# Performance work log

Hardware: AMD Instinct MI355X
Metric: run time of the kernel (lower is better)

Reference implementation:

```python
import jax, jax.numpy as jnp
import numpy as np

B, T, HID, NH = 2, 2048, 1024, 16
HD = HID // NH  # head_dim = 64
ROPE_BASE = 1000000.0


def _precompute_freqs(dim, end, rope_base):
    inv = 1.0 / (rope_base ** (np.arange(0, dim, 2)[: dim // 2].astype(np.float32) / dim))
    t = np.arange(end, dtype=np.float32)
    freqs = np.outer(t, inv).astype(np.float32)  # (end, dim//2)
    cos = np.concatenate([np.cos(freqs), np.cos(freqs)], axis=-1)
    sin = np.concatenate([np.sin(freqs), np.sin(freqs)], axis=-1)
    return jnp.asarray(cos), jnp.asarray(sin)


def setup_inputs() -> dict:
    key = jax.random.key(0)
    ks = jax.random.split(key, 5)
    x = jax.random.normal(ks[0], (B, T, HID), dtype=jnp.float32)
    s = 1.0 / np.sqrt(HID)
    Wq = jax.random.normal(ks[1], (HID, HID), dtype=jnp.float32) * s
    Wk = jax.random.normal(ks[2], (HID, HID), dtype=jnp.float32) * s
    Wv = jax.random.normal(ks[3], (HID, HID), dtype=jnp.float32) * s
    Wo = jax.random.normal(ks[4], (HID, HID), dtype=jnp.float32) * s
    cos, sin = _precompute_freqs(HD, T, ROPE_BASE)
    return {"x": x, "Wq": Wq, "Wk": Wk, "Wv": Wv, "Wo": Wo, "cos": cos, "sin": sin}


def _rotate_half(u):
    half = u.shape[-1] // 2
    return jnp.concatenate([-u[..., half:], u[..., :half]], axis=-1)


def reference(x, Wq, Wk, Wv, Wo, cos, sin):
    b, t, _ = x.shape
    # projections (nn.Linear: x @ W.T)
    q = (x @ Wq.T).reshape(b, t, NH, HD).transpose(0, 2, 1, 3)  # (B,H,T,D)
    k = (x @ Wk.T).reshape(b, t, NH, HD).transpose(0, 2, 1, 3)
    v = (x @ Wv.T).reshape(b, t, NH, HD).transpose(0, 2, 1, 3)
    c = cos[None, None, :t, :]
    s = sin[None, None, :t, :]
    q = q * c + _rotate_half(q) * s
    k = k * c + _rotate_half(k) * s
    scores = jnp.einsum("bhqd,bhkd->bhqk", q, k) / jnp.sqrt(jnp.float32(HD))
    causal = jnp.tril(jnp.ones((t, t), dtype=bool))
    scores = jnp.where(causal[None, None], scores, jnp.float32(-jnp.inf))
    prob = jax.nn.softmax(scores, axis=-1)
    out = jnp.einsum("bhqk,bhkd->bhqd", prob, v)
    out = out.transpose(0, 2, 1, 3).reshape(b, t, HID)
    return out @ Wo.T
```

## Files before the change

kernel.cpp:

```cpp
#include <hip/hip_runtime.h>
#include <hip/hip_bf16.h>

#define B_   2
#define T_   2048
#define HID_ 1024
#define NH_  16
#define HD_  64
#define K_   1024
#define M_   (B_*T_)

typedef __attribute__((ext_vector_type(8)))  short bf16x8;
typedef __attribute__((ext_vector_type(4)))  float f32x4;
typedef __attribute__((ext_vector_type(16))) float f32x16;
typedef __attribute__((ext_vector_type(4)))  unsigned int u32x4;
typedef __attribute__((ext_vector_type(2)))  unsigned int u32x2;

#define LOG2E 1.44269504088896340736f

__device__ inline unsigned short f2bf(float f) {
    __hip_bfloat16 h = __float2bfloat16(f);
    return __builtin_bit_cast(unsigned short, h);
}
__device__ inline unsigned int pk2(float a, float b) {
    return (unsigned int)f2bf(a) | ((unsigned int)f2bf(b) << 16);
}
__device__ inline unsigned int pkt(float a, float b) {
    return __builtin_amdgcn_perm(__builtin_bit_cast(unsigned, a),
                                 __builtin_bit_cast(unsigned, b), 0x03020706u);
}
__device__ inline bf16x8 cvt8(float4 a, float4 b) {
    bf16x8 r;
    r[0]=(short)f2bf(a.x); r[1]=(short)f2bf(a.y); r[2]=(short)f2bf(a.z); r[3]=(short)f2bf(a.w);
    r[4]=(short)f2bf(b.x); r[5]=(short)f2bf(b.y); r[6]=(short)f2bf(b.z); r[7]=(short)f2bf(b.w);
    return r;
}

__global__ __launch_bounds__(256)
void cast_all(const float* __restrict__ x,
              const float* __restrict__ W0, const float* __restrict__ W1,
              const float* __restrict__ W2, const float* __restrict__ W3,
              unsigned short* __restrict__ xo,
              unsigned short* __restrict__ o0, unsigned short* __restrict__ o1,
              unsigned short* __restrict__ o2, unsigned short* __restrict__ o3) {
    const int blk = blockIdx.x;
    const float* in;
    unsigned short* out;
    int i;
    if (blk < 2048) {
        in = x; out = xo; i = blk * 256 + threadIdx.x;
    } else {
        const int wb = blk - 2048, sec = wb >> 9;
        in  = (sec == 0) ? W0 : (sec == 1) ? W1 : (sec == 2) ? W2 : W3;
        out = (sec == 0) ? o0 : (sec == 1) ? o1 : (sec == 2) ? o2 : o3;
        i = (wb & 511) * 256 + threadIdx.x;
    }
    float4 a = ((const float4*)in)[2*i], b = ((const float4*)in)[2*i + 1];
    ((bf16x8*)out)[i] = cvt8(a, b);
}

template<int TYPE>
__global__ __launch_bounds__(256)
void gemm_k(const unsigned short* __restrict__ A, const unsigned short* __restrict__ W0,
            const unsigned short* __restrict__ W1, const unsigned short* __restrict__ W2,
            const float* __restrict__ cs, const float* __restrict__ sn,
            unsigned short* __restrict__ qb, unsigned short* __restrict__ kb,
            unsigned short* __restrict__ vtb, float* __restrict__ fout) {
    __shared__ unsigned short As[128*64];
    __shared__ unsigned short Bs[128*64];
    const int tid = threadIdx.x;
    const int w = tid >> 6, lane = tid & 63;
    const int u = lane >> 4, c = lane & 15;
    const int bm = blockIdx.x * 128, bn = blockIdx.y * 128;
    const int wm = (w & 1) * 64, wn = (w >> 1) * 64;
    const int srow = tid >> 3, scol = (tid & 7) << 3;

    const unsigned short* Wsec;
    int wrowbase;
    if constexpr (TYPE == 0) {
        const int sec = bn >> 10;
        Wsec = (sec == 0) ? W0 : ((sec == 1) ? W1 : W2);
        wrowbase = bn & 1023;
    } else {
        Wsec = W0;
        wrowbase = bn;
    }
    const unsigned short* Wp = Wsec + (size_t)(wrowbase + srow) * K_ + scol;
    const unsigned short* Ap = A + (size_t)(bm + srow) * K_ + scol;

    f32x4 acc[4][4] = {};
    bf16x8 ra[4], rb[4];

    auto loadin = [&](int k0) {
        #pragma unroll
        for (int i = 0; i < 4; ++i) {
            ra[i] = *(const bf16x8*)(Ap + (size_t)i * 32 * K_ + k0);
            rb[i] = *(const bf16x8*)(Wp + (size_t)i * 32 * K_ + k0);
        }
    };
    loadin(0);

    for (int k0 = 0; k0 < K_; k0 += 64) {
        __syncthreads();
        #pragma unroll
        for (int i = 0; i < 4; ++i) {
            const int row = i * 32 + srow;
            const int sc = (scol * 2) ^ ((row & 7) << 4);
            *(bf16x8*)((char*)As + row * 128 + sc) = ra[i];
            *(bf16x8*)((char*)Bs + row * 128 + sc) = rb[i];
        }
        __syncthreads();
        if (k0 < K_ - 64) loadin(k0 + 64);
        #pragma unroll
        for (int kk = 0; kk < 2; ++kk) {
            bf16x8 af[4], bfr[4];
            #pragma unroll
            for (int mi = 0; mi < 4; ++mi) {
                const int row = wm + mi * 16 + c;
                const int sc = (kk * 64 + u * 16) ^ ((row & 7) << 4);
                af[mi] = *(const bf16x8*)((char*)As + row * 128 + sc);
            }
            #pragma unroll
            for (int ni = 0; ni < 4; ++ni) {
                const int row = wn + ni * 16 + c;
                const int sc = (kk * 64 + u * 16) ^ ((row & 7) << 4);
                bfr[ni] = *(const bf16x8*)((char*)Bs + row * 128 + sc);
            }
            #pragma unroll
            for (int mi = 0; mi < 4; ++mi)
                #pragma unroll
                for (int ni = 0; ni < 4; ++ni)
                    acc[mi][ni] = __builtin_amdgcn_mfma_f32_16x16x32_bf16(
                        af[mi], bfr[ni], acc[mi][ni], 0, 0, 0);
        }
    }

    if constexpr (TYPE == 1) {
        #pragma unroll
        for (int mi = 0; mi < 4; ++mi)
            #pragma unroll
            for (int ni = 0; ni < 4; ++ni)
                #pragma unroll
                for (int r = 0; r < 4; ++r)
                    fout[(size_t)(bm + wm + 16*mi + 4*u + r) * HID_ + (bn + wn + 16*ni + c)] =
                        acc[mi][ni][r];
    } else {
        const int sec = bn >> 10;
        const int h = ((bn + wn) & 1023) >> 6;
        if (sec == 2) {
            #pragma unroll
            for (int mi = 0; mi < 4; ++mi)
                #pragma unroll
                for (int r = 0; r < 4; ++r) {
                    const int mg = bm + wm + 16*mi + 4*u + r;
                    const int bb = mg >> 11, t = mg & 2047;
                    const int tk = (t & ~12) | ((t & 4) << 1) | ((t & 8) >> 1);
                    #pragma unroll
                    for (int ni = 0; ni < 4; ++ni)
                        vtb[((size_t)(bb*16 + h) * 64 + 16*ni + c) * 2048 + tk] =
                            f2bf(acc[mi][ni][r]);
                }
        } else {
            unsigned short* ob = sec ? kb : qb;
            const float qsc = sec ? 1.0f : (0.125f * LOG2E);
            #pragma unroll
            for (int mi = 0; mi < 4; ++mi)
                #pragma unroll
                for (int r = 0; r < 4; ++r) {
                    const int mg = bm + wm + 16*mi + 4*u + r;
                    const int bb = mg >> 11, t = mg & 2047;
                    const size_t base = ((size_t)(bb*16 + h) * 2048 + t) * 64;
                    #pragma unroll
                    for (int ni = 0; ni < 2; ++ni) {
                        const int dlo = 16*ni + c;
                        const float cv = cs[t*64 + dlo], sv = sn[t*64 + dlo];
                        const float Aa = acc[mi][ni][r], Bb = acc[mi][ni+2][r];
                        ob[base + dlo]      = f2bf((Aa*cv - Bb*sv) * qsc);
                        ob[base + dlo + 32] = f2bf((Bb*cv + Aa*sv) * qsc);
                    }
                }
        }
    }
}

__global__ __launch_bounds__(256)
void attn11(const unsigned short* __restrict__ q, const unsigned short* __restrict__ k,
            const unsigned short* __restrict__ vt, unsigned short* __restrict__ ab) {
    const int raw = blockIdx.x;
    const int bh   = (raw & 7) + 8 * ((raw >> 3) & 3);
    const int qblk = 63 - (raw >> 5);
    const int tid = threadIdx.x;
    const int wid = tid >> 6, lane = tid & 63;
    const int h = lane >> 5, c = lane & 31;
    const int b = bh >> 4, hh = bh & 15;
    const int q0 = qblk * 32;
    const int qgc = q0 + c;
    const unsigned short* qp = q  + (size_t)bh * (T_*64);
    const unsigned short* kp = k  + (size_t)bh * (T_*64);
    const unsigned short* vp = vt + (size_t)bh * (64*T_);

    const int kloff  = c * 64 + 8 * h;
    const int vloff0 = c * 2048 + 8 * h;
    const int vloff1 = vloff0 + 32 * 2048;

    bf16x8 qf[4];
    {
        const unsigned short* qrow = qp + (q0 + c) * 64 + 8 * h;
        #pragma unroll
        for (int s = 0; s < 4; ++s)
            qf[s] = *(const bf16x8*)(qrow + s * 16);
    }

    f32x16 O0 = {}, O1 = {};
    float m = -1e30f, lsum = 0.f;
    const int nst = qblk + 1;

    auto loadKV = [&](bf16x8 (&kf)[4], bf16x8 (&vf)[4], int st) {
        const unsigned short* kst = kp + (st << 11);
        const unsigned short* vst = vp + (st << 5);
        #pragma unroll
        for (int s = 0; s < 4; ++s)
            kf[s] = *(const bf16x8*)(kst + kloff + s * 16);
        vf[0] = *(const bf16x8*)(vst + vloff0);
        vf[1] = *(const bf16x8*)(vst + vloff0 + 16);
        vf[2] = *(const bf16x8*)(vst + vloff1);
        vf[3] = *(const bf16x8*)(vst + vloff1 + 16);
    };

    auto process = [&](const bf16x8 (&kf)[4], const bf16x8 (&vf)[4], int st) {
        const int kvs = st << 5;
        __builtin_amdgcn_s_setprio(1);
        f32x16 sa = {};
        #pragma unroll
        for (int s = 0; s < 4; ++s)
            sa = __builtin_amdgcn_mfma_f32_32x32x16_bf16(kf[s], qf[s], sa, 0, 0, 0);
        __builtin_amdgcn_s_setprio(0);
        float p[16];
        #pragma unroll
        for (int r = 0; r < 16; ++r) p[r] = sa[r];
        if (st == qblk) {
            #pragma unroll
            for (int r = 0; r < 16; ++r) {
                const int kk = kvs + (r & 3) + 8 * (r >> 2) + 4 * h;
                if (kk > qgc) p[r] = -1e30f;
            }
        }
        const float a0 = fmaxf(fmaxf(p[0],  p[1]),  p[2]);
        const float a1 = fmaxf(fmaxf(p[3],  p[4]),  p[5]);
        const float a2 = fmaxf(fmaxf(p[6],  p[7]),  p[8]);
        const float a3 = fmaxf(fmaxf(p[9],  p[10]), p[11]);
        const float a4 = fmaxf(fmaxf(p[12], p[13]), p[14]);
        float mx = fmaxf(fmaxf(fmaxf(a0, a1), fmaxf(a2, a3)), fmaxf(a4, p[15]));
        if (!__all(mx <= m + 8.0f)) {
            mx = fmaxf(mx, __shfl_xor(mx, 32));
            const float mn = fmaxf(m, mx);
            const float f = __builtin_amdgcn_exp2f(m - mn);
            m = mn;
            lsum *= f;
            #pragma unroll
            for (int r = 0; r < 16; ++r) { O0[r] *= f; O1[r] *= f; }
        }
        float ps = 0.f;
        #pragma unroll
        for (int r = 0; r < 16; ++r) {
            p[r] = __builtin_amdgcn_exp2f(p[r] - m);
            ps += p[r];
        }
        lsum += ps;
        u32x4 B0w = { pkt(p[0],  p[1]),  pkt(p[2],  p[3]),
                      pkt(p[4],  p[5]),  pkt(p[6],  p[7])  };
        u32x4 B1w = { pkt(p[8],  p[9]),  pkt(p[10], p[11]),
                      pkt(p[12], p[13]), pkt(p[14], p[15]) };
        bf16x8 PB0 = __builtin_bit_cast(bf16x8, B0w);
        bf16x8 PB1 = __builtin_bit_cast(bf16x8, B1w);
        __builtin_amdgcn_s_setprio(1);
        O0 = __builtin_amdgcn_mfma_f32_32x32x16_bf16(vf[0], PB0, O0, 0, 0, 0);
        O0 = __builtin_amdgcn_mfma_f32_32x32x16_bf16(vf[1], PB1, O0, 0, 0, 0);
        O1 = __builtin_amdgcn_mfma_f32_32x32x16_bf16(vf[2], PB0, O1, 0, 0, 0);
        O1 = __builtin_amdgcn_mfma_f32_32x32x16_bf16(vf[3], PB1, O1, 0, 0, 0);
        __builtin_amdgcn_s_setprio(0);
    };

    bf16x8 kA[4], kB[4], vA[4], vB[4];
    if (wid < nst) loadKV(kA, vA, wid);
    for (int st = wid; st < nst; st += 8) {
        if (st + 4 < nst) loadKV(kB, vB, st + 4);
        process(kA, vA, st);
        if (st + 4 >= nst) break;
        if (st + 8 < nst) loadKV(kA, vA, st + 8);
        process(kB, vB, st + 4);
    }
    lsum += __shfl_xor(lsum, 32);

    __shared__ unsigned OSu[4][32 * 34];
    __shared__ float mS[4][32], lS[4][32];
    if (h == 0) { mS[wid][c] = m; lS[wid][c] = lsum; }
    {
        unsigned* os = &OSu[wid][0];
        const int rb = c * 34 + 2 * h;
        #pragma unroll
        for (int j = 0; j < 4; ++j) {
            os[rb + 4*j]          = pk2(O0[4*j],   O0[4*j+1]);
            os[rb + 4*j + 1]      = pk2(O0[4*j+2], O0[4*j+3]);
            os[rb + 16 + 4*j]     = pk2(O1[4*j],   O1[4*j+1]);
            os[rb + 16 + 4*j + 1] = pk2(O1[4*j+2], O1[4*j+3]);
        }
    }
    __syncthreads();

    const int ql = tid & 31, ug = (tid >> 5) * 4;
    const float M = fmaxf(fmaxf(mS[0][ql], mS[1][ql]), fmaxf(mS[2][ql], mS[3][ql]));
    float acc[8] = {};
    float L = 0.f;
    #pragma unroll
    for (int w2 = 0; w2 < 4; ++w2) {
        const float sc = __builtin_amdgcn_exp2f(mS[w2][ql] - M);
        L += lS[w2][ql] * sc;
        u32x2 pa = *(u32x2*)&OSu[w2][ql * 34 + ug];
        u32x2 pb = *(u32x2*)&OSu[w2][ql * 34 + ug + 2];
        #pragma unroll
        for (int t = 0; t < 2; ++t) {
            acc[2*t]     += __builtin_bit_cast(float, pa[t] << 16) * sc;
            acc[2*t+1]   += __builtin_bit_cast(float, pa[t] & 0xffff0000u) * sc;
            acc[4+2*t]   += __builtin_bit_cast(float, pb[t] << 16) * sc;
            acc[4+2*t+1] += __builtin_bit_cast(float, pb[t] & 0xffff0000u) * sc;
        }
    }
    const float inv = 1.0f / L;
    uint4 ov;
    ov.x = pk2(acc[0]*inv, acc[1]*inv);
    ov.y = pk2(acc[2]*inv, acc[3]*inv);
    ov.z = pk2(acc[4]*inv, acc[5]*inv);
    ov.w = pk2(acc[6]*inv, acc[7]*inv);
    *(uint4*)(ab + ((size_t)(b * T_) + q0 + ql) * HID_ + hh * 64 + ug * 2) = ov;
}

extern "C" void kernel_launch(void* const* d_in, const int* in_sizes, int n_in,
                              void* d_out, int out_size, void* d_ws, size_t ws_size,
                              hipStream_t stream) {
    const float* x  = (const float*)d_in[0];
    const float* Wq = (const float*)d_in[1];
    const float* Wk = (const float*)d_in[2];
    const float* Wv = (const float*)d_in[3];
    const float* Wo = (const float*)d_in[4];
    const float* cs = (const float*)d_in[5];
    const float* sn = (const float*)d_in[6];
    char* wsb = (char*)d_ws;
    unsigned short* xb  = (unsigned short*)(wsb);
    unsigned short* wqb = (unsigned short*)(wsb + (8u  << 20));
    unsigned short* wkb = (unsigned short*)(wsb + (10u << 20));
    unsigned short* wvb = (unsigned short*)(wsb + (12u << 20));
    unsigned short* wob = (unsigned short*)(wsb + (14u << 20));
    unsigned short* qb  = (unsigned short*)(wsb + (16u << 20));
    unsigned short* kb  = (unsigned short*)(wsb + (24u << 20));
    unsigned short* vtb = (unsigned short*)(wsb + (32u << 20));
    unsigned short* ab  = (unsigned short*)(wsb + (40u << 20));

    cast_all<<<4096, 256, 0, stream>>>(x, Wq, Wk, Wv, Wo, xb, wqb, wkb, wvb, wob);

    gemm_k<0><<<dim3(M_/128, 3072/128), 256, 0, stream>>>(
        xb, wqb, wkb, wvb, cs, sn, qb, kb, vtb, nullptr);
    attn11<<<2048, 256, 0, stream>>>(qb, kb, vtb, ab);
    gemm_k<1><<<dim3(M_/128, HID_/128), 256, 0, stream>>>(
        ab, wob, nullptr, nullptr, nullptr, nullptr,
        nullptr, nullptr, nullptr, (float*)d_out);
}
```

Before: 127.8 us.

## Process two 32-row query tiles per attention block to reuse K/V loads

The attention kernel now handles 64 query rows per block, as two 32-row sub-tiles A and B, instead of 32. Each K/V tile loaded into registers feeds both sub-tiles, with causal skipping for the A half, and the grid shrinks from 2048 to 1024 blocks. This halves global K/V traffic per query row and amortises the merge epilogue. In exchange it roughly doubles accumulator register pressure, which may reduce occupancy, and there are fewer blocks to balance the causal workload.

```diff
diff --git a/kernel.cpp b/kernel.cpp
--- a/kernel.cpp
+++ b/kernel.cpp
@@ -183,17 +183,19 @@
 }
 
 __global__ __launch_bounds__(256)
-void attn11(const unsigned short* __restrict__ q, const unsigned short* __restrict__ k,
+void attn12(const unsigned short* __restrict__ q, const unsigned short* __restrict__ k,
             const unsigned short* __restrict__ vt, unsigned short* __restrict__ ab) {
     const int raw = blockIdx.x;
-    const int bh   = (raw & 7) + 8 * ((raw >> 3) & 3);
-    const int qblk = 63 - (raw >> 5);
+    const int bh     = (raw & 7) + 8 * ((raw >> 3) & 3);
+    const int qchunk = 31 - (raw >> 5);
     const int tid = threadIdx.x;
     const int wid = tid >> 6, lane = tid & 63;
     const int h = lane >> 5, c = lane & 31;
     const int b = bh >> 4, hh = bh & 15;
-    const int q0 = qblk * 32;
-    const int qgc = q0 + c;
+    const int q0 = qchunk * 64;
+    const int qgcA = q0 + c, qgcB = q0 + 32 + c;
+    const int stAd = 2 * qchunk;
+    const int NT   = 2 * qchunk + 2;
     const unsigned short* qp = q  + (size_t)bh * (T_*64);
     const unsigned short* kp = k  + (size_t)bh * (T_*64);
     const unsigned short* vp = vt + (size_t)bh * (64*T_);
@@ -202,17 +204,19 @@
     const int vloff0 = c * 2048 + 8 * h;
     const int vloff1 = vloff0 + 32 * 2048;
 
-    bf16x8 qf[4];
+    bf16x8 qfA[4], qfB[4];
     {
-        const unsigned short* qrow = qp + (q0 + c) * 64 + 8 * h;
-        #pragma unroll
-        for (int s = 0; s < 4; ++s)
-            qf[s] = *(const bf16x8*)(qrow + s * 16);
-    }
-
-    f32x16 O0 = {}, O1 = {};
-    float m = -1e30f, lsum = 0.f;
-    const int nst = qblk + 1;
+        const unsigned short* qrowA = qp + (q0 + c) * 64 + 8 * h;
+        const unsigned short* qrowB = qrowA + 32 * 64;
+        #pragma unroll
+        for (int s = 0; s < 4; ++s) {
+            qfA[s] = *(const bf16x8*)(qrowA + s * 16);
+            qfB[s] = *(const bf16x8*)(qrowB + s * 16);
+        }
+    }
+
+    f32x16 OA0 = {}, OA1 = {}, OB0 = {}, OB1 = {};
+    float mA = -1e30f, lA = 0.f, mB = -1e30f, lB = 0.f;
 
     auto loadKV = [&](bf16x8 (&kf)[4], bf16x8 (&vf)[4], int st) {
         const unsigned short* kst = kp + (st << 11);
@@ -228,110 +232,184 @@
 
     auto process = [&](const bf16x8 (&kf)[4], const bf16x8 (&vf)[4], int st) {
         const int kvs = st << 5;
-        __builtin_amdgcn_s_setprio(1);
-        f32x16 sa = {};
-        #pragma unroll
-        for (int s = 0; s < 4; ++s)
-            sa = __builtin_amdgcn_mfma_f32_32x32x16_bf16(kf[s], qf[s], sa, 0, 0, 0);
-        __builtin_amdgcn_s_setprio(0);
-        float p[16];
-        #pragma unroll
-        for (int r = 0; r < 16; ++r) p[r] = sa[r];
-        if (st == qblk) {
+        const bool doA = (st <= stAd);
+        float pA[16], pB[16];
+        float mxA = -1e30f, mxB;
+        if (doA) {
+            __builtin_amdgcn_s_setprio(1);
+            f32x16 sa = {};
+            #pragma unroll
+            for (int s = 0; s < 4; ++s)
+                sa = __builtin_amdgcn_mfma_f32_32x32x16_bf16(kf[s], qfA[s], sa, 0, 0, 0);
+            __builtin_amdgcn_s_setprio(0);
+            #pragma unroll
+            for (int r = 0; r < 16; ++r) pA[r] = sa[r];
+            if (st == stAd) {
+                #pragma unroll
+                for (int r = 0; r < 16; ++r) {
+                    const int kk = kvs + (r & 3) + 8 * (r >> 2) + 4 * h;
+                    if (kk > qgcA) pA[r] = -1e30f;
+                }
+            }
+            const float a0 = fmaxf(fmaxf(pA[0],  pA[1]),  pA[2]);
+            const float a1 = fmaxf(fmaxf(pA[3],  pA[4]),  pA[5]);
+            const float a2 = fmaxf(fmaxf(pA[6],  pA[7]),  pA[8]);
+            const float a3 = fmaxf(fmaxf(pA[9],  pA[10]), pA[11]);
+            const float a4 = fmaxf(fmaxf(pA[12], pA[13]), pA[14]);
+            mxA = fmaxf(fmaxf(fmaxf(a0, a1), fmaxf(a2, a3)), fmaxf(a4, pA[15]));
+        }
+        {
+            __builtin_amdgcn_s_setprio(1);
+            f32x16 sa = {};
+            #pragma unroll
+            for (int s = 0; s < 4; ++s)
+                sa = __builtin_amdgcn_mfma_f32_32x32x16_bf16(kf[s], qfB[s], sa, 0, 0, 0);
+            __builtin_amdgcn_s_setprio(0);
+            #pragma unroll
+            for (int r = 0; r < 16; ++r) pB[r] = sa[r];
+            if (st == NT - 1) {
+                #pragma unroll
+                for (int r = 0; r < 16; ++r) {
+                    const int kk = kvs + (r & 3) + 8 * (r >> 2) + 4 * h;
+                    if (kk > qgcB) pB[r] = -1e30f;
+                }
+            }
+            const float a0 = fmaxf(fmaxf(pB[0],  pB[1]),  pB[2]);
+            const float a1 = fmaxf(fmaxf(pB[3],  pB[4]),  pB[5]);
+            const float a2 = fmaxf(fmaxf(pB[6],  pB[7]),  pB[8]);
+            const float a3 = fmaxf(fmaxf(pB[9],  pB[10]), pB[11]);
+            const float a4 = fmaxf(fmaxf(pB[12], pB[13]), pB[14]);
+            mxB = fmaxf(fmaxf(fmaxf(a0, a1), fmaxf(a2, a3)), fmaxf(a4, pB[15]));
+        }
+        if (!__all(fmaxf(mxA - mA, mxB - mB) <= 8.0f)) {
+            if (doA) {
+                const float fx = fmaxf(mxA, __shfl_xor(mxA, 32));
+                const float mn = fmaxf(mA, fx);
+                const float f = __builtin_amdgcn_exp2f(mA - mn);
+                mA = mn; lA *= f;
+                #pragma unroll
+                for (int r = 0; r < 16; ++r) { OA0[r] *= f; OA1[r] *= f; }
+            }
+            {
+                const float fx = fmaxf(mxB, __shfl_xor(mxB, 32));
+                const float mn = fmaxf(mB, fx);
+                const float f = __builtin_amdgcn_exp2f(mB - mn);
+                mB = mn; lB *= f;
+                #pragma unroll
+                for (int r = 0; r < 16; ++r) { OB0[r] *= f; OB1[r] *= f; }
+            }
+        }
+        if (doA) {
+            float ps = 0.f;
             #pragma unroll
             for (int r = 0; r < 16; ++r) {
-                const int kk = kvs + (r & 3) + 8 * (r >> 2) + 4 * h;
-                if (kk > qgc) p[r] = -1e30f;
-            }
-        }
-        const float a0 = fmaxf(fmaxf(p[0],  p[1]),  p[2]);
-        const float a1 = fmaxf(fmaxf(p[3],  p[4]),  p[5]);
-        const float a2 = fmaxf(fmaxf(p[6],  p[7]),  p[8]);
-        const float a3 = fmaxf(fmaxf(p[9],  p[10]), p[11]);
-        const float a4 = fmaxf(fmaxf(p[12], p[13]), p[14]);
-        float mx = fmaxf(fmaxf(fmaxf(a0, a1), fmaxf(a2, a3)), fmaxf(a4, p[15]));
-        if (!__all(mx <= m + 8.0f)) {
-            mx = fmaxf(mx, __shfl_xor(mx, 32));
-            const float mn = fmaxf(m, mx);
-            const float f = __builtin_amdgcn_exp2f(m - mn);
-            m = mn;
-            lsum *= f;
-            #pragma unroll
-            for (int r = 0; r < 16; ++r) { O0[r] *= f; O1[r] *= f; }
-        }
-        float ps = 0.f;
-        #pragma unroll
-        for (int r = 0; r < 16; ++r) {
-            p[r] = __builtin_amdgcn_exp2f(p[r] - m);
-            ps += p[r];
-        }
-        lsum += ps;
-        u32x4 B0w = { pkt(p[0],  p[1]),  pkt(p[2],  p[3]),
-                      pkt(p[4],  p[5]),  pkt(p[6],  p[7])  };
-        u32x4 B1w = { pkt(p[8],  p[9]),  pkt(p[10], p[11]),
-                      pkt(p[12], p[13]), pkt(p[14], p[15]) };
-        bf16x8 PB0 = __builtin_bit_cast(bf16x8, B0w);
-        bf16x8 PB1 = __builtin_bit_cast(bf16x8, B1w);
-        __builtin_amdgcn_s_setprio(1);
-        O0 = __builtin_amdgcn_mfma_f32_32x32x16_bf16(vf[0], PB0, O0, 0, 0, 0);
-        O0 = __builtin_amdgcn_mfma_f32_32x32x16_bf16(vf[1], PB1, O0, 0, 0, 0);
-        O1 = __builtin_amdgcn_mfma_f32_32x32x16_bf16(vf[2], PB0, O1, 0, 0, 0);
-        O1 = __builtin_amdgcn_mfma_f32_32x32x16_bf16(vf[3], PB1, O1, 0, 0, 0);
-        __builtin_amdgcn_s_setprio(0);
+                pA[r] = __builtin_amdgcn_exp2f(pA[r] - mA);
+                ps += pA[r];
+            }
+            lA += ps;
+            u32x4 B0w = { pkt(pA[0],  pA[1]),  pkt(pA[2],  pA[3]),
+                          pkt(pA[4],  pA[5]),  pkt(pA[6],  pA[7])  };
+            u32x4 B1w = { pkt(pA[8],  pA[9]),  pkt(pA[10], pA[11]),
+                          pkt(pA[12], pA[13]), pkt(pA[14], pA[15]) };
+            bf16x8 PB0 = __builtin_bit_cast(bf16x8, B0w);
+            bf16x8 PB1 = __builtin_bit_cast(bf16x8, B1w);
+            __builtin_amdgcn_s_setprio(1);
+            OA0 = __builtin_amdgcn_mfma_f32_32x32x16_bf16(vf[0], PB0, OA0, 0, 0, 0);
+            OA0 = __builtin_amdgcn_mfma_f32_32x32x16_bf16(vf[1], PB1, OA0, 0, 0, 0);
+            OA1 = __builtin_amdgcn_mfma_f32_32x32x16_bf16(vf[2], PB0, OA1, 0, 0, 0);
+            OA1 = __builtin_amdgcn_mfma_f32_32x32x16_bf16(vf[3], PB1, OA1, 0, 0, 0);
+            __builtin_amdgcn_s_setprio(0);
+        }
+        {
+            float ps = 0.f;
+            #pragma unroll
+            for (int r = 0; r < 16; ++r) {
+                pB[r] = __builtin_amdgcn_exp2f(pB[r] - mB);
+                ps += pB[r];
+            }
+            lB += ps;
+            u32x4 B0w = { pkt(pB[0],  pB[1]),  pkt(pB[2],  pB[3]),
+                          pkt(pB[4],  pB[5]),  pkt(pB[6],  pB[7])  };
+            u32x4 B1w = { pkt(pB[8],  pB[9]),  pkt(pB[10], pB[11]),
+                          pkt(pB[12], pB[13]), pkt(pB[14], pB[15]) };
+            bf16x8 PB0 = __builtin_bit_cast(bf16x8, B0w);
+            bf16x8 PB1 = __builtin_bit_cast(bf16x8, B1w);
+            __builtin_amdgcn_s_setprio(1);
+            OB0 = __builtin_amdgcn_mfma_f32_32x32x16_bf16(vf[0], PB0, OB0, 0, 0, 0);
+            OB0 = __builtin_amdgcn_mfma_f32_32x32x16_bf16(vf[1], PB1, OB0, 0, 0, 0);
+            OB1 = __builtin_amdgcn_mfma_f32_32x32x16_bf16(vf[2], PB0, OB1, 0, 0, 0);
+            OB1 = __builtin_amdgcn_mfma_f32_32x32x16_bf16(vf[3], PB1, OB1, 0, 0, 0);
+            __builtin_amdgcn_s_setprio(0);
+        }
     };
 
-    bf16x8 kA[4], kB[4], vA[4], vB[4];
-    if (wid < nst) loadKV(kA, vA, wid);
-    for (int st = wid; st < nst; st += 8) {
-        if (st + 4 < nst) loadKV(kB, vB, st + 4);
-        process(kA, vA, st);
-        if (st + 4 >= nst) break;
-        if (st + 8 < nst) loadKV(kA, vA, st + 8);
-        process(kB, vB, st + 4);
-    }
-    lsum += __shfl_xor(lsum, 32);
-
-    __shared__ unsigned OSu[4][32 * 34];
-    __shared__ float mS[4][32], lS[4][32];
-    if (h == 0) { mS[wid][c] = m; lS[wid][c] = lsum; }
+    bf16x8 kA_[4], kB_[4], vA_[4], vB_[4];
+    if (wid < NT) loadKV(kA_, vA_, wid);
+    for (int st = wid; st < NT; st += 8) {
+        if (st + 4 < NT) loadKV(kB_, vB_, st + 4);
+        process(kA_, vA_, st);
+        if (st + 4 >= NT) break;
+        if (st + 8 < NT) loadKV(kA_, vA_, st + 8);
+        process(kB_, vB_, st + 4);
+    }
+    lA += __shfl_xor(lA, 32);
+    lB += __shfl_xor(lB, 32);
+
+    __shared__ unsigned OSu[4][64 * 34];
+    __shared__ float mS[4][64], lS[4][64];
+    if (h == 0) {
+        mS[wid][c] = mA;      lS[wid][c] = lA;
+        mS[wid][32 + c] = mB; lS[wid][32 + c] = lB;
+    }
     {
         unsigned* os = &OSu[wid][0];
-        const int rb = c * 34 + 2 * h;
+        const int rbA = c * 34 + 2 * h;
+        const int rbB = (32 + c) * 34 + 2 * h;
         #pragma unroll
         for (int j = 0; j < 4; ++j) {
-            os[rb + 4*j]          = pk2(O0[4*j],   O0[4*j+1]);
-            os[rb + 4*j + 1]      = pk2(O0[4*j+2], O0[4*j+3]);
-            os[rb + 16 + 4*j]     = pk2(O1[4*j],   O1[4*j+1]);
-            os[rb + 16 + 4*j + 1] = pk2(O1[4*j+2], O1[4*j+3]);
+            os[rbA + 4*j]          = pk2(OA0[4*j],   OA0[4*j+1]);
+            os[rbA + 4*j + 1]      = pk2(OA0[4*j+2], OA0[4*j+3]);
+            os[rbA + 16 + 4*j]     = pk2(OA1[4*j],   OA1[4*j+1]);
+            os[rbA + 16 + 4*j + 1] = pk2(OA1[4*j+2], OA1[4*j+3]);
+            os[rbB + 4*j]          = pk2(OB0[4*j],   OB0[4*j+1]);
+            os[rbB + 4*j + 1]      = pk2(OB0[4*j+2], OB0[4*j+3]);
+            os[rbB + 16 + 4*j]     = pk2(OB1[4*j],   OB1[4*j+1]);
+            os[rbB + 16 + 4*j + 1] = pk2(OB1[4*j+2], OB1[4*j+3]);
         }
     }
     __syncthreads();
 
-    const int ql = tid & 31, ug = (tid >> 5) * 4;
+    const int ql = tid & 63, ug = (tid >> 6) * 8;
     const float M = fmaxf(fmaxf(mS[0][ql], mS[1][ql]), fmaxf(mS[2][ql], mS[3][ql]));
-    float acc[8] = {};
+    float acc[16] = {};
     float L = 0.f;
     #pragma unroll
     for (int w2 = 0; w2 < 4; ++w2) {
         const float sc = __builtin_amdgcn_exp2f(mS[w2][ql] - M);
         L += lS[w2][ql] * sc;
-        u32x2 pa = *(u32x2*)&OSu[w2][ql * 34 + ug];
-        u32x2 pb = *(u32x2*)&OSu[w2][ql * 34 + ug + 2];
-        #pragma unroll
-        for (int t = 0; t < 2; ++t) {
+        u32x4 pa = *(u32x4*)&OSu[w2][ql * 34 + ug];
+        u32x4 pb = *(u32x4*)&OSu[w2][ql * 34 + ug + 4];
+        #pragma unroll
+        for (int t = 0; t < 4; ++t) {
             acc[2*t]     += __builtin_bit_cast(float, pa[t] << 16) * sc;
             acc[2*t+1]   += __builtin_bit_cast(float, pa[t] & 0xffff0000u) * sc;
-            acc[4+2*t]   += __builtin_bit_cast(float, pb[t] << 16) * sc;
-            acc[4+2*t+1] += __builtin_bit_cast(float, pb[t] & 0xffff0000u) * sc;
+            acc[8+2*t]   += __builtin_bit_cast(float, pb[t] << 16) * sc;
+            acc[8+2*t+1] += __builtin_bit_cast(float, pb[t] & 0xffff0000u) * sc;
         }
     }
     const float inv = 1.0f / L;
-    uint4 ov;
-    ov.x = pk2(acc[0]*inv, acc[1]*inv);
-    ov.y = pk2(acc[2]*inv, acc[3]*inv);
-    ov.z = pk2(acc[4]*inv, acc[5]*inv);
-    ov.w = pk2(acc[6]*inv, acc[7]*inv);
-    *(uint4*)(ab + ((size_t)(b * T_) + q0 + ql) * HID_ + hh * 64 + ug * 2) = ov;
+    uint4 ov0, ov1;
+    ov0.x = pk2(acc[0]*inv,  acc[1]*inv);
+    ov0.y = pk2(acc[2]*inv,  acc[3]*inv);
+    ov0.z = pk2(acc[4]*inv,  acc[5]*inv);
+    ov0.w = pk2(acc[6]*inv,  acc[7]*inv);
+    ov1.x = pk2(acc[8]*inv,  acc[9]*inv);
+    ov1.y = pk2(acc[10]*inv, acc[11]*inv);
+    ov1.z = pk2(acc[12]*inv, acc[13]*inv);
+    ov1.w = pk2(acc[14]*inv, acc[15]*inv);
+    unsigned short* orow = ab + ((size_t)(b * T_) + q0 + ql) * HID_ + hh * 64 + ug * 2;
+    *(uint4*)orow       = ov0;
+    *(uint4*)(orow + 8) = ov1;
 }
 
 extern "C" void kernel_launch(void* const* d_in, const int* in_sizes, int n_in,
@@ -359,7 +437,7 @@
 
     gemm_k<0><<<dim3(M_/128, 3072/128), 256, 0, stream>>>(
         xb, wqb, wkb, wvb, cs, sn, qb, kb, vtb, nullptr);
-    attn11<<<2048, 256, 0, stream>>>(qb, kb, vtb, ab);
+    attn12<<<1024, 256, 0, stream>>>(qb, kb, vtb, ab);
     gemm_k<1><<<dim3(M_/128, HID_/128), 256, 0, stream>>>(
         ab, wob, nullptr, nullptr, nullptr, nullptr,
         nullptr, nullptr, nullptr, (float*)d_out);
```

Result: faster. 121.5 us (-4.9%).
